# Kernel tuning notes

Hardware: AMD Instinct MI355X
Metric: run time of the kernel (lower is better)

Reference implementation:

```python
import jax, jax.numpy as jnp
import numpy as np

# fastmax config (scalar flags fused into the original CUDA kernel)
MASK = True          # causal masking
DROPOUT = 0.1        # dropout noise scale
NORMALIZE = True     # l2-normalize q and k
TEMPERATURE = 1.0    # score temperature


def setup_inputs() -> dict:
    key = jax.random.key(0)
    ks = jax.random.split(key, 5)
    b, h, n, d = 4, 16, 1024, 64
    q = jax.random.normal(ks[0], (b, h, n, d), jnp.float32)
    k = jax.random.normal(ks[1], (b, h, n, d), jnp.float32)
    v = jax.random.normal(ks[2], (b, h, n, d), jnp.float32)
    drop_noise = jax.random.normal(ks[3], (b, h, n, d), jnp.float32)
    rpe_matrix = jax.random.normal(ks[4], (2 * n - 1, d), jnp.float32)
    return {"q": q, "k": k, "v": v, "drop_noise": drop_noise, "rpe_matrix": rpe_matrix}


def _fastmax(q, k, v, drop_noise, rpe_matrix):
    # fastmax: first-order Taylor linearization of softmax attention,
    # a_ij = (1 + q_i.k_j/t + q_i.rpe[i-j+n-1]/t) / sum_j(...), with causal
    # masking done by zeroing scores (not -inf) and dropout noise fused in.
    b, h, n, d = q.shape
    if NORMALIZE:
        q = q / jnp.linalg.norm(q, axis=-1, keepdims=True)
        k = k / jnp.linalg.norm(k, axis=-1, keepdims=True)
    # dropout noise fused into values
    v = v + DROPOUT * drop_noise
    # base Taylor scores: 1 + qk/t  -> [b,h,n,n]
    scores = 1.0 + jnp.einsum('bhid,bhjd->bhij', q, k) / TEMPERATURE
    # relative positional encoding bias: q_i . rpe[i-j+n-1]
    qr = jnp.einsum('bhid,rd->bhir', q, rpe_matrix)           # [b,h,n,2n-1]
    idx = jnp.arange(n)
    rel = idx[:, None] - idx[None, :] + (n - 1)               # [n,n] in [0, 2n-2]
    bias = jnp.take_along_axis(qr, jnp.broadcast_to(rel, (b, h, n, n)), axis=-1)
    scores = scores + bias / TEMPERATURE
    if MASK:
        causal = (idx[:, None] >= idx[None, :]).astype(scores.dtype)  # [n,n]
        scores = scores * causal
    denom = jnp.sum(scores, axis=-1, keepdims=True)           # [b,h,n,1]
    out = jnp.einsum('bhij,bhjd->bhid', scores, v) / denom
    return out


def reference(q, k, v, drop_noise, rpe_matrix):
    return _fastmax(q, k, v, drop_noise, rpe_matrix)
```

## Files before the change

### kernel.cpp

```cpp
#include <hip/hip_runtime.h>


constexpr int N   = 1024;
constexpr int D   = 64;
constexpr int NBH = 64;
constexpr int LDT = 72;

constexpr size_t KH_OFF = 0;
constexpr size_t KL_OFF = KH_OFF + (size_t)NBH * N * D * 2;
constexpr size_t VH_OFF = KL_OFF + (size_t)NBH * N * D * 2;
constexpr size_t VL_OFF = VH_OFF + (size_t)NBH * N * D * 2;
constexpr size_t RH_OFF = VL_OFF + (size_t)NBH * N * D * 2;
constexpr size_t RL_OFF = RH_OFF + (size_t)2048 * D * 2;

typedef short short8  __attribute__((ext_vector_type(8)));
typedef float float4v __attribute__((ext_vector_type(4)));

#define LDS_FENCE() asm volatile("s_waitcnt lgkmcnt(0)" ::: "memory")

__device__ __forceinline__ ushort f2bf(float x) {
    union { float f; unsigned u; } un; un.f = x;
    unsigned r = un.u + 0x7fffu + ((un.u >> 16) & 1u);
    return (ushort)(r >> 16);
}
__device__ __forceinline__ float bf2f(ushort h) {
    union { unsigned u; float f; } un; un.u = ((unsigned)h) << 16;
    return un.f;
}
__device__ __forceinline__ void split2(float x, ushort& h, ushort& l) {
    h = f2bf(x);
    l = f2bf(x - bf2f(h));
}
__device__ __forceinline__ void pack16(const float* v, ushort* dh, ushort* dl) {
    ushort hh[16], ll[16];
#pragma unroll
    for (int j = 0; j < 16; ++j) split2(v[j], hh[j], ll[j]);
    uint4 a, b;
    a.x = hh[0] | (hh[1] << 16);  a.y = hh[2] | (hh[3] << 16);
    a.z = hh[4] | (hh[5] << 16);  a.w = hh[6] | (hh[7] << 16);
    b.x = hh[8] | (hh[9] << 16);  b.y = hh[10] | (hh[11] << 16);
    b.z = hh[12] | (hh[13] << 16); b.w = hh[14] | (hh[15] << 16);
    ((uint4*)dh)[0] = a; ((uint4*)dh)[1] = b;
    a.x = ll[0] | (ll[1] << 16);  a.y = ll[2] | (ll[3] << 16);
    a.z = ll[4] | (ll[5] << 16);  a.w = ll[6] | (ll[7] << 16);
    b.x = ll[8] | (ll[9] << 16);  b.y = ll[10] | (ll[11] << 16);
    b.z = ll[12] | (ll[13] << 16); b.w = ll[14] | (ll[15] << 16);
    ((uint4*)dl)[0] = a; ((uint4*)dl)[1] = b;
}

__global__ __launch_bounds__(256) void prep_fused(
        const float* __restrict__ kg, const float* __restrict__ vg,
        const float* __restrict__ ng, const float* __restrict__ rg,
        ushort* __restrict__ kh, ushort* __restrict__ kl,
        ushort* __restrict__ vh, ushort* __restrict__ vl,
        ushort* __restrict__ rh, ushort* __restrict__ rl) {
    __shared__ ushort Th[64 * 72], Tl[64 * 72];
    const int bx = blockIdx.x;
    const int by = blockIdx.y;

    if (bx < 16) {
        const int bh = by;
        const int row = bx * 64 + (threadIdx.x >> 2);
        const int seg = threadIdx.x & 3;
        const float4* p = (const float4*)(kg + ((size_t)bh * N + row) * D + seg * 16);
        float4 f[4] = {p[0], p[1], p[2], p[3]};
        float ss = 0.f;
#pragma unroll
        for (int i = 0; i < 4; ++i)
            ss += f[i].x * f[i].x + f[i].y * f[i].y + f[i].z * f[i].z + f[i].w * f[i].w;
        ss += __shfl_xor(ss, 1, 4);
        ss += __shfl_xor(ss, 2, 4);
        const float rn = rsqrtf(ss);
        float v[16];
#pragma unroll
        for (int i = 0; i < 4; ++i) {
            v[4 * i + 0] = f[i].x * rn; v[4 * i + 1] = f[i].y * rn;
            v[4 * i + 2] = f[i].z * rn; v[4 * i + 3] = f[i].w * rn;
        }
        const size_t o = ((size_t)bh * N + row) * D + seg * 16;
        pack16(v, kh + o, kl + o);
    } else if (bx < 32) {
        const int bh = by, c0 = (bx - 16) * 64;
        const int cl = threadIdx.x >> 2, seg = threadIdx.x & 3;
        {
            const float4* pv = (const float4*)(vg + ((size_t)bh * N + c0 + cl) * D + seg * 16);
            const float4* pn = (const float4*)(ng + ((size_t)bh * N + c0 + cl) * D + seg * 16);
#pragma unroll
            for (int i = 0; i < 4; ++i) {
                float4 fv = pv[i], fn = pn[i];
                float va[4] = {fv.x + 0.1f * fn.x, fv.y + 0.1f * fn.y,
                               fv.z + 0.1f * fn.z, fv.w + 0.1f * fn.w};
#pragma unroll
                for (int j = 0; j < 4; ++j) {
                    ushort hh, ll;
                    split2(va[j], hh, ll);
                    const int dc = seg * 16 + i * 4 + j;
                    Th[dc * 72 + cl] = hh;
                    Tl[dc * 72 + cl] = ll;
                }
            }
        }
        __syncthreads();
        {
            const int dc = threadIdx.x >> 2;
            const size_t o = ((size_t)bh * D + dc) * N + c0 + seg * 16;
            uint4* sh = (uint4*)&Th[dc * 72 + seg * 16];
            uint4* sl = (uint4*)&Tl[dc * 72 + seg * 16];
            ((uint4*)(vh + o))[0] = sh[0]; ((uint4*)(vh + o))[1] = sh[1];
            ((uint4*)(vl + o))[0] = sl[0]; ((uint4*)(vl + o))[1] = sl[1];
        }
    } else {
        if (by >= 32) return;
        const int row = by * 64 + (threadIdx.x >> 2);
        if (row >= 2 * N - 1) return;
        const int seg = threadIdx.x & 3;
        const float4* p = (const float4*)(rg + (size_t)row * D + seg * 16);
        float4 f[4] = {p[0], p[1], p[2], p[3]};
        float v[16];
#pragma unroll
        for (int i = 0; i < 4; ++i) {
            v[4 * i + 0] = f[i].x; v[4 * i + 1] = f[i].y;
            v[4 * i + 2] = f[i].z; v[4 * i + 3] = f[i].w;
        }
        const size_t o = (size_t)row * D + seg * 16;
        pack16(v, rh + o, rl + o);
    }
}

__device__ __forceinline__ float4v mfma6(short8 ah0, short8 ah1, short8 al0, short8 al1,
                                         const ushort* ph, const ushort* pl, float4v c) {
    short8 bh0 = *(const short8*)ph;
    short8 bh1 = *(const short8*)(ph + 32);
    short8 bl0 = *(const short8*)pl;
    short8 bl1 = *(const short8*)(pl + 32);
    c = __builtin_amdgcn_mfma_f32_16x16x32_bf16(ah0, bh0, c, 0, 0, 0);
    c = __builtin_amdgcn_mfma_f32_16x16x32_bf16(ah1, bh1, c, 0, 0, 0);
    c = __builtin_amdgcn_mfma_f32_16x16x32_bf16(ah0, bl0, c, 0, 0, 0);
    c = __builtin_amdgcn_mfma_f32_16x16x32_bf16(ah1, bl1, c, 0, 0, 0);
    c = __builtin_amdgcn_mfma_f32_16x16x32_bf16(al0, bh0, c, 0, 0, 0);
    c = __builtin_amdgcn_mfma_f32_16x16x32_bf16(al1, bh1, c, 0, 0, 0);
    return c;
}

#define PREFETCH(i0loc, jtv) do {                                         \
    const int j0_   = (jtv) * 64;                                         \
    const int rel0_ = (i0loc) - j0_ + N - 64;                             \
    const ushort* gKh_ = khb + (size_t)j0_ * D;                           \
    const ushort* gKl_ = klb + (size_t)j0_ * D;                           \
    const ushort* gVh_ = vhb + j0_;                                       \
    const ushort* gVl_ = vlb + j0_;                                       \
    const ushort* gRh_ = rh + (size_t)rel0_ * D;                          \
    const ushort* gRl_ = rl + (size_t)rel0_ * D;                          \
    pKh0 = *(const uint4*)&gKh_[r0 * D + c8];                             \
    pKh1 = *(const uint4*)&gKh_[(r0 + 32) * D + c8];                      \
    pKl0 = *(const uint4*)&gKl_[r0 * D + c8];                             \
    pKl1 = *(const uint4*)&gKl_[(r0 + 32) * D + c8];                      \
    pVh0 = *(const uint4*)&gVh_[(size_t)r0 * N + c8];                     \
    pVh1 = *(const uint4*)&gVh_[(size_t)(r0 + 32) * N + c8];              \
    pVl0 = *(const uint4*)&gVl_[(size_t)r0 * N + c8];                     \
    pVl1 = *(const uint4*)&gVl_[(size_t)(r0 + 32) * N + c8];              \
    pRh0 = *(const uint4*)&gRh_[r0 * D + c8];                             \
    pRh1 = *(const uint4*)&gRh_[(r0 + 32) * D + c8];                      \
    pRh2 = *(const uint4*)&gRh_[(r0 + 64) * D + c8];                      \
    pRh3 = *(const uint4*)&gRh_[(r0 + 96) * D + c8];                      \
    pRl0 = *(const uint4*)&gRl_[r0 * D + c8];                             \
    pRl1 = *(const uint4*)&gRl_[(r0 + 32) * D + c8];                      \
    pRl2 = *(const uint4*)&gRl_[(r0 + 64) * D + c8];                      \
    pRl3 = *(const uint4*)&gRl_[(r0 + 96) * D + c8];                      \
} while (0)

#define STAGE_WRITE() do {                                                \
    *(uint4*)&Kh[r0 * LDT + c8]        = pKh0;                            \
    *(uint4*)&Kh[(r0 + 32) * LDT + c8] = pKh1;                            \
    *(uint4*)&Kl[r0 * LDT + c8]        = pKl0;                            \
    *(uint4*)&Kl[(r0 + 32) * LDT + c8] = pKl1;                            \
    *(uint4*)&Vh[r0 * LDT + c8]        = pVh0;                            \
    *(uint4*)&Vh[(r0 + 32) * LDT + c8] = pVh1;                            \
    *(uint4*)&Vl[r0 * LDT + c8]        = pVl0;                            \
    *(uint4*)&Vl[(r0 + 32) * LDT + c8] = pVl1;                            \
    *(uint4*)&Rh[r0 * LDT + c8]        = pRh0;                            \
    *(uint4*)&Rh[(r0 + 32) * LDT + c8] = pRh1;                            \
    *(uint4*)&Rh[(r0 + 64) * LDT + c8] = pRh2;                            \
    *(uint4*)&Rh[(r0 + 96) * LDT + c8] = pRh3;                            \
    *(uint4*)&Rl[r0 * LDT + c8]        = pRl0;                            \
    *(uint4*)&Rl[(r0 + 32) * LDT + c8] = pRl1;                            \
    *(uint4*)&Rl[(r0 + 64) * LDT + c8] = pRl2;                            \
    *(uint4*)&Rl[(r0 + 96) * LDT + c8] = pRl3;                            \
} while (0)

__global__ __launch_bounds__(256, 2)
void fastmax_main(const float* __restrict__ qg,
                  const ushort* __restrict__ kh, const ushort* __restrict__ kl,
                  const ushort* __restrict__ vh, const ushort* __restrict__ vl,
                  const ushort* __restrict__ rh, const ushort* __restrict__ rl,
                  float* __restrict__ og) {
    __shared__ __align__(16) char smem[73728];
    ushort* Kh = (ushort*)smem;
    ushort* Kl = Kh + 64 * LDT;
    ushort* Rh = Kl + 64 * LDT;
    ushort* Rl = Rh + 128 * LDT;
    ushort* Vh = Rl + 128 * LDT;
    ushort* Vl = Vh + 64 * LDT;

    const int tid  = threadIdx.x;
    const int lane = tid & 63;
    const int wv   = tid >> 6;
    const int bh   = blockIdx.y;
    const int x    = lane & 15;
    const int quad = lane >> 4;
    const int band = wv * 16;
    const int r0   = tid >> 3;
    const int c8   = (tid & 7) * 8;

    float*  Bst = (float*)(smem + wv * 5760);
    ushort* Sh  = (ushort*)(smem + wv * 5760);
    ushort* Sl  = Sh + 16 * LDT;

    const ushort* khb = kh + (size_t)bh * N * D;
    const ushort* klb = kl + (size_t)bh * N * D;
    const ushort* vhb = vh + (size_t)bh * D * N;
    const ushort* vlb = vl + (size_t)bh * D * N;

    uint4 pKh0, pKh1, pKl0, pKl1, pVh0, pVh1, pVl0, pVl1;
    uint4 pRh0, pRh1, pRh2, pRh3, pRl0, pRl1, pRl2, pRl3;

    for (int half = 0; half < 2; ++half) {
        const int bix = half == 0 ? (int)blockIdx.x + 8 : 7 - (int)blockIdx.x;
        const int i0  = bix * 64;

        const float* qrow = qg + ((size_t)bh * N + i0 + band + x) * D;
        float qf[16];
        *(float4*)&qf[0]  = *(const float4*)(qrow + quad * 8);
        *(float4*)&qf[4]  = *(const float4*)(qrow + quad * 8 + 4);
        *(float4*)&qf[8]  = *(const float4*)(qrow + 32 + quad * 8);
        *(float4*)&qf[12] = *(const float4*)(qrow + 32 + quad * 8 + 4);
        float ss = 0.f;
#pragma unroll
        for (int j = 0; j < 16; ++j) ss += qf[j] * qf[j];
        ss += __shfl_xor(ss, 16);
        ss += __shfl_xor(ss, 32);
        const float rn = rsqrtf(ss);
        short8 qh0, ql0, qh1, ql1;
#pragma unroll
        for (int j = 0; j < 8; ++j) {
            ushort h, l;
            split2(qf[j] * rn, h, l);      qh0[j] = (short)h; ql0[j] = (short)l;
            split2(qf[8 + j] * rn, h, l);  qh1[j] = (short)h; ql1[j] = (short)l;
        }

        float4v oacc[4];
#pragma unroll
        for (int i = 0; i < 4; ++i) oacc[i] = (float4v){0.f, 0.f, 0.f, 0.f};
        float pden[4] = {0.f, 0.f, 0.f, 0.f};

        if (half == 0) PREFETCH(i0, 0);

        for (int jt = 0; jt <= bix; ++jt) {
            STAGE_WRITE();
            __syncthreads();

            if (jt < bix) {
                PREFETCH(i0, jt + 1);
            } else if (half == 0) {
                const int i0n = (7 - (int)blockIdx.x) * 64;
                PREFETCH(i0n, 0);
            }

            __builtin_amdgcn_s_setprio(1);
            float4v sacc[4];
#pragma unroll
            for (int nt = 0; nt < 4; ++nt) {
                const int off = (nt * 16 + x) * LDT + quad * 8;
                float4v c = (float4v){0.f, 0.f, 0.f, 0.f};
                sacc[nt] = mfma6(qh0, qh1, ql0, ql1, &Kh[off], &Kl[off], c);
            }
            float4v racc[5];
#pragma unroll
            for (int t = 0; t < 5; ++t) {
                const int off = (band + t * 16 + x) * LDT + quad * 8;
                float4v c = (float4v){0.f, 0.f, 0.f, 0.f};
                racc[t] = mfma6(qh0, qh1, ql0, ql1, &Rh[off], &Rl[off], c);
            }
            __builtin_amdgcn_s_setprio(0);
            __syncthreads();

#pragma unroll
            for (int t = 0; t < 5; ++t) {
                float* p = &Bst[(t * 16 + x) * 18 + quad * 4];
                float2 a; a.x = racc[t][0]; a.y = racc[t][1];
                float2 b; b.x = racc[t][2]; b.y = racc[t][3];
                *(float2*)p = a;
                *(float2*)(p + 2) = b;
            }
            LDS_FENCE();

            const bool diag = (jt == bix);
            float s[4][4];
#pragma unroll
            for (int nt = 0; nt < 4; ++nt) {
#pragma unroll
                for (int rr = 0; rr < 4; ++rr) {
                    const int rt = band + quad * 4 + rr;
                    const int ct = nt * 16 + x;
                    const int wl = rt - ct + 63 - band;
                    float val = sacc[nt][rr] + Bst[wl * 18 + quad * 4 + rr] + 1.0f;
                    if (diag && ct > rt) val = 0.f;
                    pden[rr] += val;
                    s[nt][rr] = val;
                }
            }
            LDS_FENCE();

#pragma unroll
            for (int nt = 0; nt < 4; ++nt)
#pragma unroll
                for (int rr = 0; rr < 4; ++rr) {
                    ushort hh, ll;
                    split2(s[nt][rr], hh, ll);
                    Sh[(quad * 4 + rr) * LDT + nt * 16 + x] = hh;
                    Sl[(quad * 4 + rr) * LDT + nt * 16 + x] = ll;
                }
            LDS_FENCE();
            const short8 sh0 = *(const short8*)&Sh[x * LDT + quad * 8];
            const short8 sh1 = *(const short8*)&Sh[x * LDT + 32 + quad * 8];
            const short8 sl0 = *(const short8*)&Sl[x * LDT + quad * 8];
            const short8 sl1 = *(const short8*)&Sl[x * LDT + 32 + quad * 8];

            __builtin_amdgcn_s_setprio(1);
#pragma unroll
            for (int nt = 0; nt < 4; ++nt) {
                const int off = (nt * 16 + x) * LDT + quad * 8;
                oacc[nt] = mfma6(sh0, sh1, sl0, sl1, &Vh[off], &Vl[off], oacc[nt]);
            }
            __builtin_amdgcn_s_setprio(0);
            __syncthreads();
        }

        float inv[4];
#pragma unroll
        for (int rr = 0; rr < 4; ++rr) {
            float d = pden[rr];
            d += __shfl_xor(d, 1, 16);
            d += __shfl_xor(d, 2, 16);
            d += __shfl_xor(d, 4, 16);
            d += __shfl_xor(d, 8, 16);
            inv[rr] = 1.0f / d;
        }
        float* outp = og + ((size_t)bh * N + i0 + band) * D;
#pragma unroll
        for (int nt = 0; nt < 4; ++nt)
#pragma unroll
            for (int rr = 0; rr < 4; ++rr)
                outp[(size_t)(quad * 4 + rr) * D + nt * 16 + x] = oacc[nt][rr] * inv[rr];
    }
}

extern "C" void kernel_launch(void* const* d_in, const int* in_sizes, int n_in,
                              void* d_out, int out_size, void* d_ws, size_t ws_size,
                              hipStream_t stream) {
    const float* q   = (const float*)d_in[0];
    const float* k   = (const float*)d_in[1];
    const float* v   = (const float*)d_in[2];
    const float* dn  = (const float*)d_in[3];
    const float* rpe = (const float*)d_in[4];
    float* out = (float*)d_out;
    char* ws = (char*)d_ws;

    ushort* kh = (ushort*)(ws + KH_OFF);
    ushort* kl = (ushort*)(ws + KL_OFF);
    ushort* vh = (ushort*)(ws + VH_OFF);
    ushort* vl = (ushort*)(ws + VL_OFF);
    ushort* rh = (ushort*)(ws + RH_OFF);
    ushort* rl = (ushort*)(ws + RL_OFF);

    prep_fused<<<dim3(33, NBH), 256, 0, stream>>>(k, v, dn, rpe, kh, kl, vh, vl, rh, rl);
    fastmax_main<<<dim3(8, NBH), 256, 0, stream>>>(q, kh, kl, vh, vl, rh, rl, out);
}
```

Before: 171.7 us.

## Drop Rl LDS staging, split paired tiles into separate blocks, raise occupancy

The rpe low-part tile is no longer staged in LDS; each wave reads its rl fragments straight from global memory. The rpe product is also reordered so the low part pairs with qh, not ql. LDS row padding shrinks from 72 to 68, with a separate 72 stride for the score staging. Shared memory drops to about 51KB, so the launch bound moves from 2 to 4 blocks per SM. The grid doubles to one query tile per block, replacing the load-balanced pair of tiles, which may bring back causal imbalance, while the direct global rl loads add latency and the 68 stride may cause LDS bank conflicts.

```diff
diff --git a/kernel.cpp b/kernel.cpp
--- a/kernel.cpp
+++ b/kernel.cpp
@@ -4,7 +4,8 @@
 constexpr int N   = 1024;
 constexpr int D   = 64;
 constexpr int NBH = 64;
-constexpr int LDT = 72;
+constexpr int LDT = 68;
+constexpr int SDT = 72;
 
 constexpr size_t KH_OFF = 0;
 constexpr size_t KL_OFF = KH_OFF + (size_t)NBH * N * D * 2;
@@ -142,6 +143,20 @@
     return c;
 }
 
+__device__ __forceinline__ float4v mfma_qr(short8 qh0, short8 qh1, short8 ql0, short8 ql1,
+                                           const ushort* ph, short8 rl0, short8 rl1,
+                                           float4v c) {
+    short8 bh0 = *(const short8*)ph;
+    short8 bh1 = *(const short8*)(ph + 32);
+    c = __builtin_amdgcn_mfma_f32_16x16x32_bf16(qh0, bh0, c, 0, 0, 0);
+    c = __builtin_amdgcn_mfma_f32_16x16x32_bf16(qh1, bh1, c, 0, 0, 0);
+    c = __builtin_amdgcn_mfma_f32_16x16x32_bf16(ql0, bh0, c, 0, 0, 0);
+    c = __builtin_amdgcn_mfma_f32_16x16x32_bf16(ql1, bh1, c, 0, 0, 0);
+    c = __builtin_amdgcn_mfma_f32_16x16x32_bf16(qh0, rl0, c, 0, 0, 0);
+    c = __builtin_amdgcn_mfma_f32_16x16x32_bf16(qh1, rl1, c, 0, 0, 0);
+    return c;
+}
+
 #define PREFETCH(i0loc, jtv) do {                                         \
     const int j0_   = (jtv) * 64;                                         \
     const int rel0_ = (i0loc) - j0_ + N - 64;                             \
@@ -150,7 +165,6 @@
     const ushort* gVh_ = vhb + j0_;                                       \
     const ushort* gVl_ = vlb + j0_;                                       \
     const ushort* gRh_ = rh + (size_t)rel0_ * D;                          \
-    const ushort* gRl_ = rl + (size_t)rel0_ * D;                          \
     pKh0 = *(const uint4*)&gKh_[r0 * D + c8];                             \
     pKh1 = *(const uint4*)&gKh_[(r0 + 32) * D + c8];                      \
     pKl0 = *(const uint4*)&gKl_[r0 * D + c8];                             \
@@ -163,10 +177,6 @@
     pRh1 = *(const uint4*)&gRh_[(r0 + 32) * D + c8];                      \
     pRh2 = *(const uint4*)&gRh_[(r0 + 64) * D + c8];                      \
     pRh3 = *(const uint4*)&gRh_[(r0 + 96) * D + c8];                      \
-    pRl0 = *(const uint4*)&gRl_[r0 * D + c8];                             \
-    pRl1 = *(const uint4*)&gRl_[(r0 + 32) * D + c8];                      \
-    pRl2 = *(const uint4*)&gRl_[(r0 + 64) * D + c8];                      \
-    pRl3 = *(const uint4*)&gRl_[(r0 + 96) * D + c8];                      \
 } while (0)
 
 #define STAGE_WRITE() do {                                                \
@@ -182,24 +192,19 @@
     *(uint4*)&Rh[(r0 + 32) * LDT + c8] = pRh1;                            \
     *(uint4*)&Rh[(r0 + 64) * LDT + c8] = pRh2;                            \
     *(uint4*)&Rh[(r0 + 96) * LDT + c8] = pRh3;                            \
-    *(uint4*)&Rl[r0 * LDT + c8]        = pRl0;                            \
-    *(uint4*)&Rl[(r0 + 32) * LDT + c8] = pRl1;                            \
-    *(uint4*)&Rl[(r0 + 64) * LDT + c8] = pRl2;                            \
-    *(uint4*)&Rl[(r0 + 96) * LDT + c8] = pRl3;                            \
 } while (0)
 
-__global__ __launch_bounds__(256, 2)
+__global__ __launch_bounds__(256, 4)
 void fastmax_main(const float* __restrict__ qg,
                   const ushort* __restrict__ kh, const ushort* __restrict__ kl,
                   const ushort* __restrict__ vh, const ushort* __restrict__ vl,
                   const ushort* __restrict__ rh, const ushort* __restrict__ rl,
                   float* __restrict__ og) {
-    __shared__ __align__(16) char smem[73728];
+    __shared__ __align__(16) char smem[52224];
     ushort* Kh = (ushort*)smem;
     ushort* Kl = Kh + 64 * LDT;
     ushort* Rh = Kl + 64 * LDT;
-    ushort* Rl = Rh + 128 * LDT;
-    ushort* Vh = Rl + 128 * LDT;
+    ushort* Vh = Rh + 128 * LDT;
     ushort* Vl = Vh + 64 * LDT;
 
     const int tid  = threadIdx.x;
@@ -214,7 +219,7 @@
 
     float*  Bst = (float*)(smem + wv * 5760);
     ushort* Sh  = (ushort*)(smem + wv * 5760);
-    ushort* Sl  = Sh + 16 * LDT;
+    ushort* Sl  = Sh + 16 * SDT;
 
     const ushort* khb = kh + (size_t)bh * N * D;
     const ushort* klb = kl + (size_t)bh * N * D;
@@ -222,137 +227,135 @@
     const ushort* vlb = vl + (size_t)bh * D * N;
 
     uint4 pKh0, pKh1, pKl0, pKl1, pVh0, pVh1, pVl0, pVl1;
-    uint4 pRh0, pRh1, pRh2, pRh3, pRl0, pRl1, pRl2, pRl3;
-
-    for (int half = 0; half < 2; ++half) {
-        const int bix = half == 0 ? (int)blockIdx.x + 8 : 7 - (int)blockIdx.x;
-        const int i0  = bix * 64;
-
-        const float* qrow = qg + ((size_t)bh * N + i0 + band + x) * D;
-        float qf[16];
-        *(float4*)&qf[0]  = *(const float4*)(qrow + quad * 8);
-        *(float4*)&qf[4]  = *(const float4*)(qrow + quad * 8 + 4);
-        *(float4*)&qf[8]  = *(const float4*)(qrow + 32 + quad * 8);
-        *(float4*)&qf[12] = *(const float4*)(qrow + 32 + quad * 8 + 4);
-        float ss = 0.f;
-#pragma unroll
-        for (int j = 0; j < 16; ++j) ss += qf[j] * qf[j];
-        ss += __shfl_xor(ss, 16);
-        ss += __shfl_xor(ss, 32);
-        const float rn = rsqrtf(ss);
-        short8 qh0, ql0, qh1, ql1;
-#pragma unroll
-        for (int j = 0; j < 8; ++j) {
-            ushort h, l;
-            split2(qf[j] * rn, h, l);      qh0[j] = (short)h; ql0[j] = (short)l;
-            split2(qf[8 + j] * rn, h, l);  qh1[j] = (short)h; ql1[j] = (short)l;
-        }
-
-        float4v oacc[4];
-#pragma unroll
-        for (int i = 0; i < 4; ++i) oacc[i] = (float4v){0.f, 0.f, 0.f, 0.f};
-        float pden[4] = {0.f, 0.f, 0.f, 0.f};
-
-        if (half == 0) PREFETCH(i0, 0);
-
-        for (int jt = 0; jt <= bix; ++jt) {
-            STAGE_WRITE();
-            __syncthreads();
-
-            if (jt < bix) {
-                PREFETCH(i0, jt + 1);
-            } else if (half == 0) {
-                const int i0n = (7 - (int)blockIdx.x) * 64;
-                PREFETCH(i0n, 0);
+    uint4 pRh0, pRh1, pRh2, pRh3;
+
+    const int bix = 15 - (int)blockIdx.x;
+    const int i0  = bix * 64;
+
+    const float* qrow = qg + ((size_t)bh * N + i0 + band + x) * D;
+    float qf[16];
+    *(float4*)&qf[0]  = *(const float4*)(qrow + quad * 8);
+    *(float4*)&qf[4]  = *(const float4*)(qrow + quad * 8 + 4);
+    *(float4*)&qf[8]  = *(const float4*)(qrow + 32 + quad * 8);
+    *(float4*)&qf[12] = *(const float4*)(qrow + 32 + quad * 8 + 4);
+    float ss = 0.f;
+#pragma unroll
+    for (int j = 0; j < 16; ++j) ss += qf[j] * qf[j];
+    ss += __shfl_xor(ss, 16);
+    ss += __shfl_xor(ss, 32);
+    const float rn = rsqrtf(ss);
+    short8 qh0, ql0, qh1, ql1;
+#pragma unroll
+    for (int j = 0; j < 8; ++j) {
+        ushort h, l;
+        split2(qf[j] * rn, h, l);      qh0[j] = (short)h; ql0[j] = (short)l;
+        split2(qf[8 + j] * rn, h, l);  qh1[j] = (short)h; ql1[j] = (short)l;
+    }
+
+    float4v oacc[4];
+#pragma unroll
+    for (int i = 0; i < 4; ++i) oacc[i] = (float4v){0.f, 0.f, 0.f, 0.f};
+    float pden[4] = {0.f, 0.f, 0.f, 0.f};
+
+    PREFETCH(i0, 0);
+
+    for (int jt = 0; jt <= bix; ++jt) {
+        STAGE_WRITE();
+        __syncthreads();
+
+        if (jt < bix) PREFETCH(i0, jt + 1);
+
+        const int rel0 = i0 - jt * 64 + N - 64;
+
+        __builtin_amdgcn_s_setprio(1);
+        float4v sacc[4];
+#pragma unroll
+        for (int nt = 0; nt < 4; ++nt) {
+            const int off = (nt * 16 + x) * LDT + quad * 8;
+            float4v c = (float4v){0.f, 0.f, 0.f, 0.f};
+            sacc[nt] = mfma6(qh0, qh1, ql0, ql1, &Kh[off], &Kl[off], c);
+        }
+        float4v racc[5];
+#pragma unroll
+        for (int t = 0; t < 5; ++t) {
+            const ushort* prl = rl + (size_t)(rel0 + band + t * 16 + x) * D + quad * 8;
+            short8 rl0 = *(const short8*)prl;
+            short8 rl1 = *(const short8*)(prl + 32);
+            const int off = (band + t * 16 + x) * LDT + quad * 8;
+            float4v c = (float4v){0.f, 0.f, 0.f, 0.f};
+            racc[t] = mfma_qr(qh0, qh1, ql0, ql1, &Rh[off], rl0, rl1, c);
+        }
+        __builtin_amdgcn_s_setprio(0);
+        __syncthreads();
+
+#pragma unroll
+        for (int t = 0; t < 5; ++t) {
+            float* p = &Bst[(t * 16 + x) * 18 + quad * 4];
+            float2 a; a.x = racc[t][0]; a.y = racc[t][1];
+            float2 b; b.x = racc[t][2]; b.y = racc[t][3];
+            *(float2*)p = a;
+            *(float2*)(p + 2) = b;
+        }
+        LDS_FENCE();
+
+        const bool diag = (jt == bix);
+        float s[4][4];
+#pragma unroll
+        for (int nt = 0; nt < 4; ++nt) {
+#pragma unroll
+            for (int rr = 0; rr < 4; ++rr) {
+                const int rt = band + quad * 4 + rr;
+                const int ct = nt * 16 + x;
+                const int wl = rt - ct + 63 - band;
+                float val = sacc[nt][rr] + Bst[wl * 18 + quad * 4 + rr] + 1.0f;
+                if (diag && ct > rt) val = 0.f;
+                pden[rr] += val;
+                s[nt][rr] = val;
             }
-
-            __builtin_amdgcn_s_setprio(1);
-            float4v sacc[4];
-#pragma unroll
-            for (int nt = 0; nt < 4; ++nt) {
-                const int off = (nt * 16 + x) * LDT + quad * 8;
-                float4v c = (float4v){0.f, 0.f, 0.f, 0.f};
-                sacc[nt] = mfma6(qh0, qh1, ql0, ql1, &Kh[off], &Kl[off], c);
+        }
+        LDS_FENCE();
+
+#pragma unroll
+        for (int nt = 0; nt < 4; ++nt)
+#pragma unroll
+            for (int rr = 0; rr < 4; ++rr) {
+                ushort hh, ll;
+                split2(s[nt][rr], hh, ll);
+                Sh[(quad * 4 + rr) * SDT + nt * 16 + x] = hh;
+                Sl[(quad * 4 + rr) * SDT + nt * 16 + x] = ll;
             }
-            float4v racc[5];
-#pragma unroll
-            for (int t = 0; t < 5; ++t) {
-                const int off = (band + t * 16 + x) * LDT + quad * 8;
-                float4v c = (float4v){0.f, 0.f, 0.f, 0.f};
-                racc[t] = mfma6(qh0, qh1, ql0, ql1, &Rh[off], &Rl[off], c);
-            }
-            __builtin_amdgcn_s_setprio(0);
-            __syncthreads();
-
-#pragma unroll
-            for (int t = 0; t < 5; ++t) {
-                float* p = &Bst[(t * 16 + x) * 18 + quad * 4];
-                float2 a; a.x = racc[t][0]; a.y = racc[t][1];
-                float2 b; b.x = racc[t][2]; b.y = racc[t][3];
-                *(float2*)p = a;
-                *(float2*)(p + 2) = b;
-            }
-            LDS_FENCE();
-
-            const bool diag = (jt == bix);
-            float s[4][4];
-#pragma unroll
-            for (int nt = 0; nt < 4; ++nt) {
-#pragma unroll
-                for (int rr = 0; rr < 4; ++rr) {
-                    const int rt = band + quad * 4 + rr;
-                    const int ct = nt * 16 + x;
-                    const int wl = rt - ct + 63 - band;
-                    float val = sacc[nt][rr] + Bst[wl * 18 + quad * 4 + rr] + 1.0f;
-                    if (diag && ct > rt) val = 0.f;
-                    pden[rr] += val;
-                    s[nt][rr] = val;
-                }
-            }
-            LDS_FENCE();
-
-#pragma unroll
-            for (int nt = 0; nt < 4; ++nt)
-#pragma unroll
-                for (int rr = 0; rr < 4; ++rr) {
-                    ushort hh, ll;
-                    split2(s[nt][rr], hh, ll);
-                    Sh[(quad * 4 + rr) * LDT + nt * 16 + x] = hh;
-                    Sl[(quad * 4 + rr) * LDT + nt * 16 + x] = ll;
-                }
-            LDS_FENCE();
-            const short8 sh0 = *(const short8*)&Sh[x * LDT + quad * 8];
-            const short8 sh1 = *(const short8*)&Sh[x * LDT + 32 + quad * 8];
-            const short8 sl0 = *(const short8*)&Sl[x * LDT + quad * 8];
-            const short8 sl1 = *(const short8*)&Sl[x * LDT + 32 + quad * 8];
-
-            __builtin_amdgcn_s_setprio(1);
-#pragma unroll
-            for (int nt = 0; nt < 4; ++nt) {
-                const int off = (nt * 16 + x) * LDT + quad * 8;
-                oacc[nt] = mfma6(sh0, sh1, sl0, sl1, &Vh[off], &Vl[off], oacc[nt]);
-            }
-            __builtin_amdgcn_s_setprio(0);
-            __syncthreads();
-        }
-
-        float inv[4];
-#pragma unroll
-        for (int rr = 0; rr < 4; ++rr) {
-            float d = pden[rr];
-            d += __shfl_xor(d, 1, 16);
-            d += __shfl_xor(d, 2, 16);
-            d += __shfl_xor(d, 4, 16);
-            d += __shfl_xor(d, 8, 16);
-            inv[rr] = 1.0f / d;
-        }
-        float* outp = og + ((size_t)bh * N + i0 + band) * D;
-#pragma unroll
-        for (int nt = 0; nt < 4; ++nt)
-#pragma unroll
-            for (int rr = 0; rr < 4; ++rr)
-                outp[(size_t)(quad * 4 + rr) * D + nt * 16 + x] = oacc[nt][rr] * inv[rr];
+        LDS_FENCE();
+        const short8 sh0 = *(const short8*)&Sh[x * SDT + quad * 8];
+        const short8 sh1 = *(const short8*)&Sh[x * SDT + 32 + quad * 8];
+        const short8 sl0 = *(const short8*)&Sl[x * SDT + quad * 8];
+        const short8 sl1 = *(const short8*)&Sl[x * SDT + 32 + quad * 8];
+
+        __builtin_amdgcn_s_setprio(1);
+#pragma unroll
+        for (int nt = 0; nt < 4; ++nt) {
+            const int off = (nt * 16 + x) * LDT + quad * 8;
+            oacc[nt] = mfma6(sh0, sh1, sl0, sl1, &Vh[off], &Vl[off], oacc[nt]);
+        }
+        __builtin_amdgcn_s_setprio(0);
+        __syncthreads();
     }
+
+    float inv[4];
+#pragma unroll
+    for (int rr = 0; rr < 4; ++rr) {
+        float d = pden[rr];
+        d += __shfl_xor(d, 1, 16);
+        d += __shfl_xor(d, 2, 16);
+        d += __shfl_xor(d, 4, 16);
+        d += __shfl_xor(d, 8, 16);
+        inv[rr] = 1.0f / d;
+    }
+    float* outp = og + ((size_t)bh * N + i0 + band) * D;
+#pragma unroll
+    for (int nt = 0; nt < 4; ++nt)
+#pragma unroll
+        for (int rr = 0; rr < 4; ++rr)
+            outp[(size_t)(quad * 4 + rr) * D + nt * 16 + x] = oacc[nt][rr] * inv[rr];
 }
 
 extern "C" void kernel_launch(void* const* d_in, const int* in_sizes, int n_in,
@@ -374,5 +377,5 @@
     ushort* rl = (ushort*)(ws + RL_OFF);
 
     prep_fused<<<dim3(33, NBH), 256, 0, stream>>>(k, v, dn, rpe, kh, kl, vh, vl, rh, rl);
-    fastmax_main<<<dim3(8, NBH), 256, 0, stream>>>(q, kh, kl, vh, vl, rh, rl, out);
-}
+    fastmax_main<<<dim3(16, NBH), 256, 0, stream>>>(q, kh, kl, vh, vl, rh, rl, out);
+}
```

Measured after the change: 477.3 us. 2.78x slower.
